# Optimization experiments

Measured on AMD Instinct MI355X. Metric: run time of the kernel, lower is better.

## Reference

```python
import jax, jax.numpy as jnp
import numpy as np

B, N, E, H, LIT, SEM, OUT = 32, 512, 128, 64, 64, 64, 64
T_FWD, T_REV = 3, 3
NEG = 1e20


def setup_inputs() -> dict:
    key = jax.random.key(0)
    ks = jax.random.split(key, 20)
    f = lambda k, sh: jax.random.normal(k, sh, dtype=jnp.float32) * 0.05
    cfg1 = jax.random.bernoulli(ks[0], 0.05, (B, N, N)).astype(jnp.float32)
    cfg2 = jax.random.bernoulli(ks[1], 0.05, (B, N, N)).astype(jnp.float32)
    return dict(
        CFG1ST=cfg1, LFG1ST=jnp.zeros((B, N, N), jnp.float32),
        LITERAL1ST=f(ks[2], (B, N, LIT)), SEMANTIC1ST=f(ks[3], (B, N, SEM)),
        CFG2ND=cfg2, LFG2ND=jnp.zeros((B, N, N), jnp.float32),
        LITERAL2ND=f(ks[4], (B, N, LIT)), SEMANTIC2ND=f(ks[5], (B, N, SEM)),
        W_lit1=f(ks[6], (LIT, H)), gru_k1=f(ks[7], (SEM, 3 * H)),
        gru_rk1=f(ks[8], (H, 3 * H)), gru_b1=jnp.zeros((2, 3 * H), jnp.float32),
        W_lit2=f(ks[9], (LIT, H)), gru_k2=f(ks[10], (SEM, 3 * H)),
        gru_rk2=f(ks[11], (H, 3 * H)), gru_b2=jnp.zeros((2, 3 * H), jnp.float32),
        a1_w=f(ks[12], (E, 1)), a1_b=jnp.zeros((1,), jnp.float32),
        a2_w=f(ks[13], (E, 1)), a2_b=jnp.zeros((1,), jnp.float32),
        W_g=f(ks[14], (E, E)),
        W_out=f(ks[15], (E, OUT)), b_out=jnp.zeros((OUT,), jnp.float32),
    )


def _gru_seq(x, k, rk, b):
    """Keras GRU (reset_after=True, tanh/sigmoid), return_sequences. x:[B,T,D] -> [B,T,H]."""
    xp = jnp.einsum('btd,dh->bth', x, k) + b[0]  # [B,T,3H]
    xz, xr, xh = jnp.split(xp, 3, axis=-1)

    h0 = jnp.zeros((x.shape[0], rk.shape[0]), x.dtype)

    def step(h, xs):
        xz_t, xr_t, xh_t = xs
        rec = h @ rk + b[1]
        rz, rr, rh = jnp.split(rec, 3, axis=-1)
        z = jax.nn.sigmoid(xz_t + rz)
        r = jax.nn.sigmoid(xr_t + rr)
        hh = jnp.tanh(xh_t + r * rh)
        h = z * h + (1.0 - z) * hh
        return h, h

    xs = (xz.transpose(1, 0, 2), xr.transpose(1, 0, 2), xh.transpose(1, 0, 2))
    _, seq = jax.lax.scan(step, h0, xs)
    return seq.transpose(1, 0, 2)


def _graph_pass(wh, A, a1_w, a1_b, a2_w, a2_b, W_g, steps):
    """GAT-like propagation. wh:[B,N,E], A:[B,N,N]."""
    mask = A * NEG - NEG  # 0 where edge, -1e20 where no edge
    for _ in range(steps):
        ah1 = wh @ a1_w + a1_b                    # [B,N,1]
        ah2 = wh @ a2_w + a2_b                    # [B,N,1]
        eij = ah1 + jnp.swapaxes(ah2, 1, 2)       # [B,N,N]
        aij = jax.nn.softmax(jax.nn.leaky_relu(eij, 0.2) + mask, axis=-1)
        attn = aij * A
        trans = jnp.einsum('bij,bjd->bid', attn, wh @ W_g)
        wh = jax.nn.elu(wh + trans)
    return wh


def reference(CFG1ST, LFG1ST, LITERAL1ST, SEMANTIC1ST,
              CFG2ND, LFG2ND, LITERAL2ND, SEMANTIC2ND,
              W_lit1, gru_k1, gru_rk1, gru_b1,
              W_lit2, gru_k2, gru_rk2, gru_b2,
              a1_w, a1_b, a2_w, a2_b, W_g, W_out, b_out):
    # TRAINING=False: dropout layers are identity.
    def data(lit, sem, Wl, k, rk, b):
        l = jax.nn.relu(lit @ Wl)                 # [B,N,H]
        s = _gru_seq(sem, k, rk, b)               # [B,N,H]
        return jnp.concatenate([l, s], axis=-1)   # [B,N,E]

    def embed(x, A):
        fwd = _graph_pass(jax.nn.relu(x), A, a1_w, a1_b, a2_w, a2_b, W_g, T_FWD)
        rev = _graph_pass(jax.nn.relu(x), jnp.swapaxes(A, 1, 2), a1_w, a1_b, a2_w, a2_b, W_g, T_REV)
        mid = jnp.sum(fwd + rev, axis=1)          # [B,E]
        return mid @ W_out + b_out                # [B,OUT]

    e1 = embed(data(LITERAL1ST, SEMANTIC1ST, W_lit1, gru_k1, gru_rk1, gru_b1), CFG1ST)
    e2 = embed(data(LITERAL2ND, SEMANTIC2ND, W_lit2, gru_k2, gru_rk2, gru_b2), CFG2ND)

    n1 = e1 / jnp.maximum(jnp.linalg.norm(e1, axis=1, keepdims=True), 1e-12)
    n2 = e2 / jnp.maximum(jnp.linalg.norm(e2, axis=1, keepdims=True), 1e-12)
    cos = jnp.sum(n1 * n2, axis=1)
    # tf cosine_similarity returns -cos; label = -(cosin - 1)/2 = (1 + cos)/2
    return (1.0 + cos) / 2.0
```

## Files before the change

### kernel.cpp

```cpp
#include <hip/hip_runtime.h>
#include <hip/hip_bf16.h>

#define BB 32
#define NNODE 512
#define EE 128
#define MAXDEG 64

typedef float v2f __attribute__((ext_vector_type(2)));
__device__ __forceinline__ v2f fma2(v2f a, v2f b, v2f c) {
  return __builtin_elementwise_fma(a, b, c);
}

__device__ __forceinline__ float sigm_fast(float x) {
  return __builtin_amdgcn_rcpf(1.0f + __expf(-x));
}
__device__ __forceinline__ float tanh_fast(float x) {
  x = fminf(20.f, fmaxf(-20.f, x));
  float t = __expf(-2.f * x);
  return (1.f - t) * __builtin_amdgcn_rcpf(1.f + t);
}

__global__ __launch_bounds__(64, 1) void k_data(
    const float* __restrict__ lit1, const float* __restrict__ sem1,
    const float* __restrict__ lit2, const float* __restrict__ sem2,
    const float* __restrict__ wl1, const float* __restrict__ gk1,
    const float* __restrict__ gb1, const float* __restrict__ wl2,
    const float* __restrict__ gk2, const float* __restrict__ gb2,
    float* __restrict__ wh, float* __restrict__ xp) {
  __shared__ float stage[64 * 65];
  int bid = blockIdx.x;
  int rowblk = bid >> 1, half = bid & 1;
  int grow0 = rowblk * 64;
  int side = grow0 >> 14;
  int lrow0 = grow0 & 16383;
  const float* lit = side ? lit2 : lit1;
  const float* sem = side ? sem2 : sem1;
  const float* wl = side ? wl2 : wl1;
  const float* gk = side ? gk2 : gk1;
  const float* gb = side ? gb2 : gb1;
  int tid = threadIdx.x;

  {
    const float4* lit4 = (const float4*)(lit + (size_t)lrow0 * 64);
#pragma unroll
    for (int p = 0; p < 16; ++p) {
      int s = p * 64 + tid;
      int r = s >> 4, q = s & 15;
      float4 v = lit4[r * 16 + q];
      stage[r * 65 + 4 * q + 0] = v.x;
      stage[r * 65 + 4 * q + 1] = v.y;
      stage[r * 65 + 4 * q + 2] = v.z;
      stage[r * 65 + 4 * q + 3] = v.w;
    }
    v2f acc[16];
#pragma unroll
    for (int c = 0; c < 16; ++c) acc[c] = (v2f){0.f, 0.f};
    const float4* wl4 = (const float4*)wl;
    for (int i = 0; i < 64; ++i) {
      float rv = stage[tid * 65 + i];
      v2f rv2 = {rv, rv};
#pragma unroll
      for (int c4 = 0; c4 < 8; ++c4) {
        float4 w = wl4[i * 16 + half * 8 + c4];
        acc[2 * c4 + 0] = fma2(rv2, (v2f){w.x, w.y}, acc[2 * c4 + 0]);
        acc[2 * c4 + 1] = fma2(rv2, (v2f){w.z, w.w}, acc[2 * c4 + 1]);
      }
    }
    float4* w0 = (float4*)wh + ((size_t)(2 * side) * 16384 + lrow0 + tid) * 32;
    float4* w1 =
        (float4*)wh + ((size_t)(2 * side + 1) * 16384 + lrow0 + tid) * 32;
#pragma unroll
    for (int c4 = 0; c4 < 8; ++c4) {
      float4 o;
      o.x = fmaxf(acc[2 * c4].x, 0.f);
      o.y = fmaxf(acc[2 * c4].y, 0.f);
      o.z = fmaxf(acc[2 * c4 + 1].x, 0.f);
      o.w = fmaxf(acc[2 * c4 + 1].y, 0.f);
      w0[half * 8 + c4] = o;
      w1[half * 8 + c4] = o;
    }
  }
  {
    const float4* sem4 = (const float4*)(sem + (size_t)lrow0 * 64);
#pragma unroll
    for (int p = 0; p < 16; ++p) {
      int s = p * 64 + tid;
      int r = s >> 4, q = s & 15;
      float4 v = sem4[r * 16 + q];
      stage[r * 65 + 4 * q + 0] = v.x;
      stage[r * 65 + 4 * q + 1] = v.y;
      stage[r * 65 + 4 * q + 2] = v.z;
      stage[r * 65 + 4 * q + 3] = v.w;
    }
    v2f acc2[48];
#pragma unroll
    for (int c = 0; c < 48; ++c)
      acc2[c] = (v2f){gb[half * 96 + 2 * c], gb[half * 96 + 2 * c + 1]};
    const float4* gk4 = (const float4*)gk;
    for (int i = 0; i < 64; ++i) {
      float rv = stage[tid * 65 + i];
      v2f rv2 = {rv, rv};
#pragma unroll
      for (int c4 = 0; c4 < 24; ++c4) {
        float4 w = gk4[i * 48 + half * 24 + c4];
        acc2[2 * c4 + 0] = fma2(rv2, (v2f){w.x, w.y}, acc2[2 * c4 + 0]);
        acc2[2 * c4 + 1] = fma2(rv2, (v2f){w.z, w.w}, acc2[2 * c4 + 1]);
      }
    }
    float4* xp4 = (float4*)xp;
    int grow = grow0 + tid;
#pragma unroll
    for (int c4 = 0; c4 < 24; ++c4) {
      float4 o;
      o.x = acc2[2 * c4].x;
      o.y = acc2[2 * c4].y;
      o.z = acc2[2 * c4 + 1].x;
      o.w = acc2[2 * c4 + 1].y;
      xp4[(size_t)grow * 48 + half * 24 + c4] = o;
    }
  }
}

__global__ __launch_bounds__(256, 1) void k_gru_cf(
    const float* __restrict__ xp, const float* __restrict__ rk1,
    const float* __restrict__ b1, const float* __restrict__ rk2,
    const float* __restrict__ b2, float* __restrict__ wh,
    const float* __restrict__ A1, const float* __restrict__ A2,
    int* __restrict__ counts, int* __restrict__ edges) {
  int tid = threadIdx.x;
  if (blockIdx.x < 64) {
    if (tid >= 64) return;
    int blk = blockIdx.x;
    int side = blk >> 5, b = blk & 31;
    int jj = tid;
    const float* rk = side ? rk2 : rk1;
    const float* bbp = side ? b2 : b1;
    v2f wz[32], wr[32], wv[32];
#pragma unroll
    for (int p = 0; p < 32; ++p) {
      const float* r0 = rk + (size_t)(2 * p) * 192 + jj;
      const float* r1 = rk + (size_t)(2 * p + 1) * 192 + jj;
      wz[p] = (v2f){r0[0], r1[0]};
      wr[p] = (v2f){r0[64], r1[64]};
      wv[p] = (v2f){r0[128], r1[128]};
    }
    float bz = bbp[192 + jj], brr = bbp[192 + 64 + jj],
          bv = bbp[192 + 128 + jj];

    __shared__ float hs[64];
    __shared__ float xpb[2][16 * 192];
    hs[jj] = 0.f;
    float hold = 0.f;

    const float* xpr = xp + (size_t)(side * 16384 + b * 512) * 192;
    float* w0 = wh + ((size_t)(2 * side) * 16384 + b * 512) * 128 + 64 + jj;
    float* w1 = wh + ((size_t)(2 * side + 1) * 16384 + b * 512) * 128 + 64 + jj;

    {
      const float4* src = (const float4*)xpr;
      float4* dst = (float4*)xpb[0];
#pragma unroll
      for (int q = 0; q < 12; ++q) dst[q * 64 + jj] = src[q * 64 + jj];
    }
    asm volatile("s_waitcnt lgkmcnt(0)" ::: "memory");

    int cur = 0;
    float hout[16];
    for (int tc = 0; tc < 32; ++tc) {
      float4 pf[12];
      if (tc + 1 < 32) {
        const float4* src = (const float4*)(xpr + (size_t)(tc + 1) * 3072);
#pragma unroll
        for (int q = 0; q < 12; ++q) pf[q] = src[q * 64 + jj];
      }
#pragma unroll
      for (int tt = 0; tt < 16; ++tt) {
        const float* xc = &xpb[cur][tt * 192];
        float cxz = xc[jj], cxr = xc[64 + jj], cxv = xc[128 + jj];
        const float4* h4 = (const float4*)hs;
        v2f az = {0.f, 0.f}, ar = {0.f, 0.f}, av = {0.f, 0.f};
#pragma unroll
        for (int c = 0; c < 16; ++c) {
          float4 h = h4[c];
          v2f hlo = {h.x, h.y}, hhi = {h.z, h.w};
          az = fma2(hlo, wz[2 * c], az);
          az = fma2(hhi, wz[2 * c + 1], az);
          ar = fma2(hlo, wr[2 * c], ar);
          ar = fma2(hhi, wr[2 * c + 1], ar);
          av = fma2(hlo, wv[2 * c], av);
          av = fma2(hhi, wv[2 * c + 1], av);
        }
        float saz = az.x + az.y, sar = ar.x + ar.y, sav = av.x + av.y;
        float z = sigm_fast(cxz + saz + bz);
        float r = sigm_fast(cxr + sar + brr);
        float hh = tanh_fast(cxv + r * (sav + bv));
        float hnew = fmaf(z, hold - hh, hh);
        hout[tt] = hnew;
        hold = hnew;
        hs[jj] = hnew;
      }
      size_t ro = (size_t)(tc * 16) * 128;
#pragma unroll
      for (int tt = 0; tt < 16; ++tt) {
        float rv = fmaxf(hout[tt], 0.f);
        w0[ro + (size_t)tt * 128] = rv;
        w1[ro + (size_t)tt * 128] = rv;
      }
      if (tc + 1 < 32) {
        float4* dst = (float4*)xpb[cur ^ 1];
#pragma unroll
        for (int q = 0; q < 12; ++q) dst[q * 64 + jj] = pf[q];
      }
      cur ^= 1;
    }
    return;
  }
  int bid = blockIdx.x - 64;
  int t = tid;
  if (bid < 512) {
    int s = bid >> 8, b = (bid >> 3) & 31, ch = bid & 7;
    const float* A = s ? A2 : A1;
    const float4* A4 = (const float4*)(A + ((size_t)b * 512 + ch * 64) * 512);
    __shared__ int crow[64];
    if (t < 64) crow[t] = 0;
    __syncthreads();
    int* efwd =
        edges + (size_t)(2 * s) * 1048576 + ((size_t)b * 512 + ch * 64) * 64;
#pragma unroll
    for (int it = 0; it < 32; ++it) {
      int idx = it * 256 + t;
      int r = idx >> 7, c4 = idx & 127;
      float4 v = A4[idx];
      float vv[4] = {v.x, v.y, v.z, v.w};
#pragma unroll
      for (int e = 0; e < 4; ++e) {
        if (vv[e] != 0.f) {
          int pos = atomicAdd(&crow[r], 1);
          if (pos < MAXDEG) efwd[r * 64 + pos] = 4 * c4 + e;
        }
      }
    }
    __syncthreads();
    if (t < 64)
      counts[(2 * s) * 16384 + b * 512 + ch * 64 + t] = min(crow[t], MAXDEG);
  } else {
    int bid2 = bid - 512;
    int s = bid2 >> 8, b = (bid2 >> 3) & 31, cch = bid2 & 7;
    const float* A = s ? A2 : A1;
    __shared__ int ccol[64];
    if (t < 64) ccol[t] = 0;
    __syncthreads();
    int lane = t & 63, rg = t >> 6;
    int c = cch * 64 + lane;
    int* erev = edges + (size_t)(2 * s + 1) * 1048576 + ((size_t)b * 512) * 64;
    const float* Ab = A + (size_t)b * 512 * 512;
    for (int it = 0; it < 128; ++it) {
      int r = it * 4 + rg;
      float a = Ab[(size_t)r * 512 + c];
      if (a != 0.f) {
        int pos = atomicAdd(&ccol[lane], 1);
        if (pos < MAXDEG) erev[(size_t)c * 64 + pos] = r;
      }
    }
    __syncthreads();
    if (t < 64)
      counts[(2 * s + 1) * 16384 + b * 512 + cch * 64 + t] =
          min(ccol[t], MAXDEG);
  }
}

__global__ __launch_bounds__(64, 1) void k_whg(
    const float* __restrict__ wh, const float* __restrict__ Wg,
    const float* __restrict__ a1w, const float* __restrict__ a1b,
    const float* __restrict__ a2w, const float* __restrict__ a2b,
    unsigned int* __restrict__ whg, float* __restrict__ ah1,
    float* __restrict__ ah2) {
  __shared__ float stage[64 * 129];
  int B = blockIdx.x;
  int xcd = B & 7, slot = B >> 3;
  int grp = xcd + 8 * (slot >> 3);
  int sub = slot & 7;
  int rowbase = grp * 512 + sub * 64;
  int tid = threadIdx.x;
  const float4* wh4 = (const float4*)(wh + (size_t)rowbase * 128);
#pragma unroll
  for (int p = 0; p < 32; ++p) {
    int s = p * 64 + tid;
    int r = s >> 5, q = s & 31;
    float4 v = wh4[r * 32 + q];
    stage[r * 129 + 4 * q + 0] = v.x;
    stage[r * 129 + 4 * q + 1] = v.y;
    stage[r * 129 + 4 * q + 2] = v.z;
    stage[r * 129 + 4 * q + 3] = v.w;
  }
  v2f acc[64];
#pragma unroll
  for (int c = 0; c < 64; ++c) acc[c] = (v2f){0.f, 0.f};
  float p1 = a1b[0], p2 = a2b[0];
  const float4* Wg4 = (const float4*)Wg;
  for (int i = 0; i < 128; ++i) {
    float rv = stage[tid * 129 + i];
    v2f rv2 = {rv, rv};
    p1 = fmaf(rv, a1w[i], p1);
    p2 = fmaf(rv, a2w[i], p2);
#pragma unroll
    for (int c4 = 0; c4 < 32; ++c4) {
      float4 w = Wg4[i * 32 + c4];
      acc[2 * c4 + 0] = fma2(rv2, (v2f){w.x, w.y}, acc[2 * c4 + 0]);
      acc[2 * c4 + 1] = fma2(rv2, (v2f){w.z, w.w}, acc[2 * c4 + 1]);
    }
  }
  int grow = rowbase + tid;
  uint2* o2 = (uint2*)(whg + (size_t)grow * 64);
#pragma unroll
  for (int c4 = 0; c4 < 32; c4 += 2) {
    __hip_bfloat162 A =
        __float22bfloat162_rn(make_float2(acc[c4].x, acc[c4].y));
    __hip_bfloat162 Bv =
        __float22bfloat162_rn(make_float2(acc[c4 + 1].x, acc[c4 + 1].y));
    uint2 pk;
    pk.x = *(unsigned int*)&A;
    pk.y = *(unsigned int*)&Bv;
    o2[c4 >> 1] = pk;
  }
  ah1[grow] = p1;
  ah2[grow] = p2;
}

__global__ __launch_bounds__(256, 1) void k_attn(
    float* __restrict__ wh, const unsigned int* __restrict__ whg,
    const float* __restrict__ ah1, const float* __restrict__ ah2,
    const int* __restrict__ counts, const int* __restrict__ edges) {
  int B = blockIdx.x;
  int xcd = B & 7, slot = B >> 3;
  int grp = xcd + 8 * (slot >> 7);
  int sub = slot & 127;
  int row = grp * 512 + sub * 4 + (threadIdx.x >> 6);
  int lane = threadIdx.x & 63;
  int st = row >> 14;
  int loc = row & 16383;
  int base = row & ~511;
  int cnt = counts[row];
  const int* ed = edges + (size_t)st * 1048576 + (size_t)loc * 64;
  int jk = lane < cnt ? ed[lane] : 0;
  float a1v = ah1[row];
  float e = a1v + ah2[base + jk];
  e = e >= 0.f ? e : 0.2f * e;
  float w = lane < cnt ? __expf(e) : 0.f;
  float lsum = w;
#pragma unroll
  for (int off = 32; off; off >>= 1) lsum += __shfl_xor(lsum, off, 64);
  float inv = cnt > 0 ? 1.0f / lsum : 0.f;
  const unsigned int* wgb = whg + (size_t)base * 64;
  v2f a0 = {0.f, 0.f}, a1 = {0.f, 0.f}, a2 = {0.f, 0.f}, a3 = {0.f, 0.f};
  int k = 0;
  for (; k + 4 <= cnt; k += 4) {
    float w0 = __shfl(w, k, 64), w1 = __shfl(w, k + 1, 64);
    float w2 = __shfl(w, k + 2, 64), w3 = __shfl(w, k + 3, 64);
    int j0 = __shfl(jk, k, 64), j1 = __shfl(jk, k + 1, 64);
    int j2 = __shfl(jk, k + 2, 64), j3 = __shfl(jk, k + 3, 64);
    unsigned int d0 = wgb[(size_t)j0 * 64 + lane];
    unsigned int d1 = wgb[(size_t)j1 * 64 + lane];
    unsigned int d2 = wgb[(size_t)j2 * 64 + lane];
    unsigned int d3 = wgb[(size_t)j3 * 64 + lane];
    v2f v0 = {__uint_as_float(d0 << 16), __uint_as_float(d0 & 0xffff0000u)};
    v2f v1 = {__uint_as_float(d1 << 16), __uint_as_float(d1 & 0xffff0000u)};
    v2f v2 = {__uint_as_float(d2 << 16), __uint_as_float(d2 & 0xffff0000u)};
    v2f v3 = {__uint_as_float(d3 << 16), __uint_as_float(d3 & 0xffff0000u)};
    a0 = fma2((v2f){w0, w0}, v0, a0);
    a1 = fma2((v2f){w1, w1}, v1, a1);
    a2 = fma2((v2f){w2, w2}, v2, a2);
    a3 = fma2((v2f){w3, w3}, v3, a3);
  }
  for (; k < cnt; ++k) {
    float w0 = __shfl(w, k, 64);
    int j0 = __shfl(jk, k, 64);
    unsigned int d0 = wgb[(size_t)j0 * 64 + lane];
    v2f v0 = {__uint_as_float(d0 << 16), __uint_as_float(d0 & 0xffff0000u)};
    a0 = fma2((v2f){w0, w0}, v0, a0);
  }
  v2f acc = (a0 + a1) + (a2 + a3);
  float2* wr2 = (float2*)(wh + (size_t)row * 128);
  float2 old = wr2[lane];
  float o0 = old.x + acc.x * inv;
  float o1 = old.y + acc.y * inv;
  o0 = o0 > 0.f ? o0 : __expf(o0) - 1.f;
  o1 = o1 > 0.f ? o1 : __expf(o1) - 1.f;
  wr2[lane] = make_float2(o0, o1);
}

__global__ __launch_bounds__(256, 1) void k_tail(const float* __restrict__ wh,
                                                 const float* __restrict__ Wout,
                                                 const float* __restrict__ bout,
                                                 float* __restrict__ e12) {
  int sb = blockIdx.x;
  int side = sb >> 5, b = sb & 31;
  int t = threadIdx.x;
  int c = t & 127, half = t >> 7;
  __shared__ float part[2][128];
  __shared__ float mid[128];
  size_t s0 = ((size_t)(2 * side) * 16384 + b * 512) * 128;
  size_t s1 = ((size_t)(2 * side + 1) * 16384 + b * 512) * 128;
  float sum = 0.f;
  int r0 = half * 256;
  for (int r = r0; r < r0 + 256; ++r) {
    sum += wh[s0 + (size_t)r * 128 + c] + wh[s1 + (size_t)r * 128 + c];
  }
  part[half][c] = sum;
  __syncthreads();
  if (t < 128) mid[t] = part[0][t] + part[1][t];
  __syncthreads();
  if (t < 64) {
    float acc = bout[t];
    for (int k2 = 0; k2 < 128; ++k2) acc = fmaf(mid[k2], Wout[k2 * 64 + t], acc);
    e12[sb * 64 + t] = acc;
  }
}

__global__ void k_cos(const float* __restrict__ e12, float* __restrict__ out) {
  int b = threadIdx.x;
  if (b >= 32) return;
  const float* e1 = e12 + b * 64;
  const float* e2 = e12 + 2048 + b * 64;
  float d = 0.f, n1 = 0.f, n2 = 0.f;
  for (int o = 0; o < 64; ++o) {
    float a = e1[o], c = e2[o];
    d = fmaf(a, c, d);
    n1 = fmaf(a, a, n1);
    n2 = fmaf(c, c, n2);
  }
  float nn = fmaxf(sqrtf(n1), 1e-12f) * fmaxf(sqrtf(n2), 1e-12f);
  out[b] = 0.5f * (1.f + d / nn);
}

extern "C" void kernel_launch(void* const* d_in, const int* in_sizes, int n_in,
                              void* d_out, int out_size, void* d_ws,
                              size_t ws_size, hipStream_t stream) {
  const float* CFG1 = (const float*)d_in[0];
  const float* LIT1 = (const float*)d_in[2];
  const float* SEM1 = (const float*)d_in[3];
  const float* CFG2 = (const float*)d_in[4];
  const float* LIT2 = (const float*)d_in[6];
  const float* SEM2 = (const float*)d_in[7];
  const float* WL1 = (const float*)d_in[8];
  const float* GK1 = (const float*)d_in[9];
  const float* GRK1 = (const float*)d_in[10];
  const float* GB1 = (const float*)d_in[11];
  const float* WL2 = (const float*)d_in[12];
  const float* GK2 = (const float*)d_in[13];
  const float* GRK2 = (const float*)d_in[14];
  const float* GB2 = (const float*)d_in[15];
  const float* A1W = (const float*)d_in[16];
  const float* A1B = (const float*)d_in[17];
  const float* A2W = (const float*)d_in[18];
  const float* A2B = (const float*)d_in[19];
  const float* WG = (const float*)d_in[20];
  const float* WOUT = (const float*)d_in[21];
  const float* BOUT = (const float*)d_in[22];

  float* ws = (float*)d_ws;
  float* wh = ws;
  float* xp = wh + 8388608;
  unsigned int* whg = (unsigned int*)(xp + 6291456);
  float* ah1 = (float*)(whg + 4194304);
  float* ah2 = ah1 + 65536;
  float* e12 = ah2 + 65536;
  int* counts = (int*)(e12 + 4096);
  int* edges = counts + 65536;

  k_data<<<1024, 64, 0, stream>>>(LIT1, SEM1, LIT2, SEM2, WL1, GK1, GB1, WL2,
                                  GK2, GB2, wh, xp);
  k_gru_cf<<<1088, 256, 0, stream>>>(xp, GRK1, GB1, GRK2, GB2, wh, CFG1, CFG2,
                                     counts, edges);
  for (int step = 0; step < 3; ++step) {
    k_whg<<<1024, 64, 0, stream>>>(wh, WG, A1W, A1B, A2W, A2B, whg, ah1, ah2);
    k_attn<<<16384, 256, 0, stream>>>(wh, whg, ah1, ah2, counts, edges);
  }
  k_tail<<<64, 256, 0, stream>>>(wh, WOUT, BOUT, e12);
  k_cos<<<1, 64, 0, stream>>>(e12, (float*)d_out);
}
```

Measured before the change: 805.5 us.

## Split GRU and CSR build into separate kernels; register-buffer GRU inputs

The fused kernel that ran the serial GRU recurrence alongside the adjacency-to-edge-list conversion is split into two launches, k_csr and k_gru, run back to back on the same stream. The GRU now prefetches input projections into register double buffers in chunks of 8 timesteps instead of staging them through shared memory. It also writes each hidden state as soon as it is computed instead of batching 16 rows. This cuts shared-memory traffic and per-chunk latency on the serial critical path, but gives up the overlap of CSR construction with the GRU, so the CSR work is now added serially.

After: 925.5 us. 1.15x slower.

```diff
diff --git a/kernel.cpp b/kernel.cpp
--- a/kernel.cpp
+++ b/kernel.cpp
@@ -121,102 +121,11 @@
   }
 }
 
-__global__ __launch_bounds__(256, 1) void k_gru_cf(
-    const float* __restrict__ xp, const float* __restrict__ rk1,
-    const float* __restrict__ b1, const float* __restrict__ rk2,
-    const float* __restrict__ b2, float* __restrict__ wh,
+__global__ __launch_bounds__(256, 1) void k_csr(
     const float* __restrict__ A1, const float* __restrict__ A2,
     int* __restrict__ counts, int* __restrict__ edges) {
-  int tid = threadIdx.x;
-  if (blockIdx.x < 64) {
-    if (tid >= 64) return;
-    int blk = blockIdx.x;
-    int side = blk >> 5, b = blk & 31;
-    int jj = tid;
-    const float* rk = side ? rk2 : rk1;
-    const float* bbp = side ? b2 : b1;
-    v2f wz[32], wr[32], wv[32];
-#pragma unroll
-    for (int p = 0; p < 32; ++p) {
-      const float* r0 = rk + (size_t)(2 * p) * 192 + jj;
-      const float* r1 = rk + (size_t)(2 * p + 1) * 192 + jj;
-      wz[p] = (v2f){r0[0], r1[0]};
-      wr[p] = (v2f){r0[64], r1[64]};
-      wv[p] = (v2f){r0[128], r1[128]};
-    }
-    float bz = bbp[192 + jj], brr = bbp[192 + 64 + jj],
-          bv = bbp[192 + 128 + jj];
-
-    __shared__ float hs[64];
-    __shared__ float xpb[2][16 * 192];
-    hs[jj] = 0.f;
-    float hold = 0.f;
-
-    const float* xpr = xp + (size_t)(side * 16384 + b * 512) * 192;
-    float* w0 = wh + ((size_t)(2 * side) * 16384 + b * 512) * 128 + 64 + jj;
-    float* w1 = wh + ((size_t)(2 * side + 1) * 16384 + b * 512) * 128 + 64 + jj;
-
-    {
-      const float4* src = (const float4*)xpr;
-      float4* dst = (float4*)xpb[0];
-#pragma unroll
-      for (int q = 0; q < 12; ++q) dst[q * 64 + jj] = src[q * 64 + jj];
-    }
-    asm volatile("s_waitcnt lgkmcnt(0)" ::: "memory");
-
-    int cur = 0;
-    float hout[16];
-    for (int tc = 0; tc < 32; ++tc) {
-      float4 pf[12];
-      if (tc + 1 < 32) {
-        const float4* src = (const float4*)(xpr + (size_t)(tc + 1) * 3072);
-#pragma unroll
-        for (int q = 0; q < 12; ++q) pf[q] = src[q * 64 + jj];
-      }
-#pragma unroll
-      for (int tt = 0; tt < 16; ++tt) {
-        const float* xc = &xpb[cur][tt * 192];
-        float cxz = xc[jj], cxr = xc[64 + jj], cxv = xc[128 + jj];
-        const float4* h4 = (const float4*)hs;
-        v2f az = {0.f, 0.f}, ar = {0.f, 0.f}, av = {0.f, 0.f};
-#pragma unroll
-        for (int c = 0; c < 16; ++c) {
-          float4 h = h4[c];
-          v2f hlo = {h.x, h.y}, hhi = {h.z, h.w};
-          az = fma2(hlo, wz[2 * c], az);
-          az = fma2(hhi, wz[2 * c + 1], az);
-          ar = fma2(hlo, wr[2 * c], ar);
-          ar = fma2(hhi, wr[2 * c + 1], ar);
-          av = fma2(hlo, wv[2 * c], av);
-          av = fma2(hhi, wv[2 * c + 1], av);
-        }
-        float saz = az.x + az.y, sar = ar.x + ar.y, sav = av.x + av.y;
-        float z = sigm_fast(cxz + saz + bz);
-        float r = sigm_fast(cxr + sar + brr);
-        float hh = tanh_fast(cxv + r * (sav + bv));
-        float hnew = fmaf(z, hold - hh, hh);
-        hout[tt] = hnew;
-        hold = hnew;
-        hs[jj] = hnew;
-      }
-      size_t ro = (size_t)(tc * 16) * 128;
-#pragma unroll
-      for (int tt = 0; tt < 16; ++tt) {
-        float rv = fmaxf(hout[tt], 0.f);
-        w0[ro + (size_t)tt * 128] = rv;
-        w1[ro + (size_t)tt * 128] = rv;
-      }
-      if (tc + 1 < 32) {
-        float4* dst = (float4*)xpb[cur ^ 1];
-#pragma unroll
-        for (int q = 0; q < 12; ++q) dst[q * 64 + jj] = pf[q];
-      }
-      cur ^= 1;
-    }
-    return;
-  }
-  int bid = blockIdx.x - 64;
-  int t = tid;
+  int bid = blockIdx.x;
+  int t = threadIdx.x;
   if (bid < 512) {
     int s = bid >> 8, b = (bid >> 3) & 31, ch = bid & 7;
     const float* A = s ? A2 : A1;
@@ -266,6 +175,84 @@
     if (t < 64)
       counts[(2 * s + 1) * 16384 + b * 512 + cch * 64 + t] =
           min(ccol[t], MAXDEG);
+  }
+}
+
+__global__ __launch_bounds__(64, 1) void k_gru(
+    const float* __restrict__ xp, const float* __restrict__ rk1,
+    const float* __restrict__ b1, const float* __restrict__ rk2,
+    const float* __restrict__ b2, float* __restrict__ wh) {
+  int blk = blockIdx.x;
+  int side = blk >> 5, b = blk & 31;
+  int jj = threadIdx.x;
+  const float* rk = side ? rk2 : rk1;
+  const float* bbp = side ? b2 : b1;
+  v2f wz[32], wr[32], wv[32];
+#pragma unroll
+  for (int p = 0; p < 32; ++p) {
+    const float* r0 = rk + (size_t)(2 * p) * 192 + jj;
+    const float* r1 = r0 + 192;
+    wz[p] = (v2f){r0[0], r1[0]};
+    wr[p] = (v2f){r0[64], r1[64]};
+    wv[p] = (v2f){r0[128], r1[128]};
+  }
+  float bz = bbp[192 + jj], brr = bbp[192 + 64 + jj], bv = bbp[192 + 128 + jj];
+
+  __shared__ float hs[64];
+  hs[jj] = 0.f;
+  float hold = 0.f;
+
+  const float* xpr = xp + (size_t)(side * 16384 + b * 512) * 192;
+  float* w0 = wh + ((size_t)(2 * side) * 16384 + b * 512) * 128 + 64 + jj;
+  float* w1 = wh + ((size_t)(2 * side + 1) * 16384 + b * 512) * 128 + 64 + jj;
+
+  float bufA[24], bufB[24];
+  auto loadc = [&](float (&buf)[24], int tc) {
+    const float* src = xpr + (size_t)tc * 8 * 192;
+#pragma unroll
+    for (int q = 0; q < 8; ++q) {
+      buf[3 * q + 0] = src[q * 192 + jj];
+      buf[3 * q + 1] = src[q * 192 + 64 + jj];
+      buf[3 * q + 2] = src[q * 192 + 128 + jj];
+    }
+  };
+  auto gstep = [&](const float (&buf)[24], int tt, int t) {
+    float cxz = buf[3 * tt + 0], cxr = buf[3 * tt + 1], cxv = buf[3 * tt + 2];
+    const float4* h4 = (const float4*)hs;
+    v2f az = {0.f, 0.f}, ar = {0.f, 0.f}, av = {0.f, 0.f};
+#pragma unroll
+    for (int c = 0; c < 16; ++c) {
+      float4 h = h4[c];
+      v2f hlo = {h.x, h.y}, hhi = {h.z, h.w};
+      az = fma2(hlo, wz[2 * c], az);
+      az = fma2(hhi, wz[2 * c + 1], az);
+      ar = fma2(hlo, wr[2 * c], ar);
+      ar = fma2(hhi, wr[2 * c + 1], ar);
+      av = fma2(hlo, wv[2 * c], av);
+      av = fma2(hhi, wv[2 * c + 1], av);
+    }
+    float saz = az.x + az.y, sar = ar.x + ar.y, sav = av.x + av.y;
+    float z = sigm_fast(cxz + saz + bz);
+    float r = sigm_fast(cxr + sar + brr);
+    float hh = tanh_fast(cxv + r * (sav + bv));
+    float hnew = fmaf(z, hold - hh, hh);
+    hold = hnew;
+    __builtin_amdgcn_sched_barrier(0);
+    hs[jj] = hnew;
+    float rv = fmaxf(hnew, 0.f);
+    w0[(size_t)t * 128] = rv;
+    w1[(size_t)t * 128] = rv;
+  };
+
+  loadc(bufA, 0);
+  for (int tc2 = 0; tc2 < 32; ++tc2) {
+    int tcA = 2 * tc2, tcB = 2 * tc2 + 1;
+    loadc(bufB, tcB);
+#pragma unroll
+    for (int tt = 0; tt < 8; ++tt) gstep(bufA, tt, tcA * 8 + tt);
+    if (tcB + 1 < 64) loadc(bufA, tcB + 1);
+#pragma unroll
+    for (int tt = 0; tt < 8; ++tt) gstep(bufB, tt, tcB * 8 + tt);
   }
 }
 
@@ -470,8 +457,8 @@
 
   k_data<<<1024, 64, 0, stream>>>(LIT1, SEM1, LIT2, SEM2, WL1, GK1, GB1, WL2,
                                   GK2, GB2, wh, xp);
-  k_gru_cf<<<1088, 256, 0, stream>>>(xp, GRK1, GB1, GRK2, GB2, wh, CFG1, CFG2,
-                                     counts, edges);
+  k_csr<<<1024, 256, 0, stream>>>(CFG1, CFG2, counts, edges);
+  k_gru<<<64, 64, 0, stream>>>(xp, GRK1, GB1, GRK2, GB2, wh);
   for (int step = 0; step < 3; ++step) {
     k_whg<<<1024, 64, 0, stream>>>(wh, WG, A1W, A1B, A2W, A2B, whg, ah1, ah2);
     k_attn<<<16384, 256, 0, stream>>>(wh, whg, ah1, ah2, counts, edges);
```
